# Performance work log

Hardware: AMD Instinct MI355X
Metric: run time of the kernel (lower is better)

## Reference

```python
import jax, jax.numpy as jnp
import numpy as np

BATCH, CHANNEL, LENGTH, CHI, D = 1024, 10, 784, 64, 2


def _dims():
    # dims[n+1] = min(d**(n+1), chi, d**(length-n-1)); dims[0] = 1
    dims = [1]
    for n in range(LENGTH):
        dims.append(min(D ** (n + 1), CHI, D ** (LENGTH - n - 1)))
    return dims


def _site_mask():
    # zero out tensor entries outside the [dims[n], dims[n+1]] bond block; this is
    # exactly equivalent to the per-site slicing in the torch code, but lets us
    # run one uniform lax.scan over sites with full-chi tensors.
    dims = _dims()
    mask = np.zeros((LENGTH, CHI, 1, CHI), np.float32)
    for n in range(LENGTH):
        mask[n, :dims[n], :, :dims[n + 1]] = 1.0
    return jnp.asarray(mask)


def setup_inputs() -> dict:
    key = jax.random.key(0)
    k1, k2 = jax.random.split(key)
    x = jax.random.uniform(k1, (BATCH, D, LENGTH), dtype=jnp.float32)
    scale = 1.0 / np.sqrt(CHI * D)
    tensors = jax.random.normal(k2, (CHANNEL, LENGTH, CHI, D, CHI), dtype=jnp.float32) * scale
    return {"x": x, "tensors": tensors}


def _forward(x, tensors):
    # mask == slicing tensors[:, nt, :dims[nt], :, :dims[nt+1]] at every site
    mt = tensors * _site_mask()[None]              # (c, L, chi, d, chi)
    A = jnp.transpose(mt, (1, 0, 2, 3, 4))         # (L, c, chi, d, chi)
    xs = jnp.transpose(x, (2, 0, 1))               # (L, n, d)
    is_last = jnp.arange(LENGTH) == LENGTH - 1
    y0 = jnp.zeros((x.shape[0], CHANNEL, CHI), x.dtype).at[:, :, 0].set(1.0)

    def step(y, inp):
        a, xv, last = inp
        y = jnp.einsum('nca,caib,ni->ncb', y, a, xv)
        # activation '(tanh(y)+1)/2' on all sites except the last one
        y = jnp.where(last, y, (jnp.tanh(y) + 1.0) * 0.5)
        return y, None

    y, _ = jax.lax.scan(step, y0, (A, xs, is_last))
    return y[:, :, :1]  # dims[length] == 1 -> (n, channel, 1)


def reference(x, tensors):
    return _forward(x, tensors)
```

## Files before the change

### kernel.cpp

```cpp
#include <hip/hip_runtime.h>
#include <hip/hip_bf16.h>


#define LEN 784
#define NCH 10

typedef short bf16x8 __attribute__((ext_vector_type(8)));
typedef float f32x4  __attribute__((ext_vector_type(4)));

#define WSA_SHORTS ((size_t)NCH * LEN * 8192)
#define WSX_FLOATS ((size_t)1024 * 2 * LEN)
#define WS_NEED (WSA_SHORTS * 2 + WSX_FLOATS * 4)

#define XSCALE -2.88539008177792681f
#define XUNDO  -0.34657359027997264f

static __device__ __forceinline__ unsigned short f2bf(float f) {
    union { __hip_bfloat16 h; unsigned short s; } u;
    u.h = __float2bfloat16(f);
    return u.s;
}

__global__ __launch_bounds__(1024) void prepass(const float* __restrict__ x,
                                                const float* __restrict__ tens,
                                                short* __restrict__ wsA,
                                                float* __restrict__ wsX)
{
    const int bid = blockIdx.x;
    const int t = threadIdx.x;
    if (bid < NCH * LEN) {
        const int w = t >> 8, ii = (t >> 7) & 1, kf = (t >> 6) & 1, l = t & 63;
        const int bout = 16 * w + (l & 15);
        const int a0 = 32 * kf + 8 * (l >> 4);
        const float* src = tens + (size_t)bid * 8192;
        unsigned int wv[4];
        #pragma unroll
        for (int p = 0; p < 4; ++p) {
            float f0 = src[(size_t)(a0 + 2 * p) * 128 + ii * 64 + bout];
            float f1 = src[(size_t)(a0 + 2 * p + 1) * 128 + ii * 64 + bout];
            wv[p] = (unsigned)f2bf(f0) | ((unsigned)f2bf(f1) << 16);
        }
        *(int4*)(wsA + (size_t)bid * 8192 + (size_t)t * 8) = *(int4*)wv;
    } else {
        int b = bid - NCH * LEN;
        if (t < LEN) {
            float v0 = x[(size_t)b * (2 * LEN) + t] * XSCALE;
            float v1 = x[(size_t)b * (2 * LEN) + LEN + t] * XSCALE;
            float2 pk; pk.x = v0; pk.y = v1;
            *(float2*)(wsX + (size_t)b * (2 * LEN) + 2 * t) = pk;
        }
    }
}

template <bool USE_WS>
__global__ __launch_bounds__(256, 3) void mps_fwd5(const float* __restrict__ x,
                                                   const float* __restrict__ tens,
                                                   const short* __restrict__ wsA,
                                                   const float* __restrict__ wsX,
                                                   float* __restrict__ out)
{
    __shared__ short tbuf[2][1024];

    const int tid = threadIdx.x;
    const int lane = tid & 63;
    const int w = tid >> 6;
    const int g = lane >> 4, l15 = lane & 15;

    const int p = blockIdx.x;
    const int gidx = (p & 7) * 80 + (p >> 3);
    const int ch = gidx >> 6;
    const int b0 = (gidx & 63) * 16;

    const short* asrc = wsA + (size_t)ch * LEN * 8192 + (size_t)w * 2048;
    const float* tsrc = tens + (size_t)ch * LEN * 8192;
    const float* xsrc = USE_WS ? (wsX + (size_t)(b0 + l15) * (2 * LEN))
                               : (x + (size_t)(b0 + l15) * (2 * LEN));

    for (int idx = tid; idx < 1024; idx += 256) {
        int col = idx >> 6, a = idx & 63;
        tbuf[0][col * 64 + 8 * ((a >> 3) ^ (col & 7)) + (a & 7)] =
            (a == 0) ? (short)0x3F80 : (short)0;
    }

    int rd_off0 = l15 * 64 + 8 * ((0 + g) ^ (l15 & 7));
    int rd_off1 = l15 * 64 + 8 * ((4 + g) ^ (l15 & 7));
    const int wr_off = l15 * 64 + 8 * ((2 * w + (g >> 1)) ^ (l15 & 7)) + 4 * (g & 1);

    auto loadA = [&](int site, bf16x8 (&A)[4]) {
        site = site < LEN ? site : LEN - 1;
        if (USE_WS) {
            const short* sb = asrc + (size_t)site * 8192;
            #pragma unroll
            for (int f = 0; f < 4; ++f)
                A[f] = *(const bf16x8*)(sb + f * 512 + lane * 8);
        } else {
            const float* sb = tsrc + (size_t)site * 8192;
            #pragma unroll
            for (int f = 0; f < 4; ++f) {
                int ii = f >> 1, kf = f & 1;
                int bout = 16 * w + l15;
                int a0 = 32 * kf + 8 * g;
                unsigned int wv[4];
                #pragma unroll
                for (int q2 = 0; q2 < 4; ++q2) {
                    float f0 = sb[(size_t)(a0 + 2 * q2) * 128 + ii * 64 + bout];
                    float f1 = sb[(size_t)(a0 + 2 * q2 + 1) * 128 + ii * 64 + bout];
                    wv[q2] = (unsigned)f2bf(f0) | ((unsigned)f2bf(f1) << 16);
                }
                A[f] = *(bf16x8*)wv;
            }
        }
    };

    auto loadX = [&](int nb, float4& qa, float4& qb) {
        nb = nb <= LEN - 4 ? nb : LEN - 4;
        if (USE_WS) {
            qa = *(const float4*)(xsrc + 2 * nb);
            qb = *(const float4*)(xsrc + 2 * nb + 4);
        } else {
            float4 xi0 = *(const float4*)(xsrc + nb);
            float4 xi1 = *(const float4*)(xsrc + LEN + nb);
            qa.x = xi0.x * XSCALE; qa.y = xi1.x * XSCALE;
            qa.z = xi0.y * XSCALE; qa.w = xi1.y * XSCALE;
            qb.x = xi0.z * XSCALE; qb.y = xi1.z * XSCALE;
            qb.z = xi0.w * XSCALE; qb.w = xi1.w * XSCALE;
        }
    };

    auto body = [&](int n, bf16x8 (&Ac)[4], bf16x8 (&Al)[4], float x0s, float x1s) {
        const int cur = n & 1, nxt = cur ^ 1;

        loadA(n + 2, Al);

        bf16x8 tf0 = *(const bf16x8*)&tbuf[cur][rd_off0];
        bf16x8 tf1 = *(const bf16x8*)&tbuf[cur][rd_off1];

        f32x4 acc0 = (f32x4){0.f, 0.f, 0.f, 0.f};
        f32x4 acc1 = (f32x4){0.f, 0.f, 0.f, 0.f};
        acc0 = __builtin_amdgcn_mfma_f32_16x16x32_bf16(Ac[0], tf0, acc0, 0, 0, 0);
        acc0 = __builtin_amdgcn_mfma_f32_16x16x32_bf16(Ac[1], tf1, acc0, 0, 0, 0);
        acc1 = __builtin_amdgcn_mfma_f32_16x16x32_bf16(Ac[2], tf0, acc1, 0, 0, 0);
        acc1 = __builtin_amdgcn_mfma_f32_16x16x32_bf16(Ac[3], tf1, acc1, 0, 0, 0);

        if (n == LEN - 1) {
            if (w == 0 && g == 0) {
                float v = (x0s * acc0[0] + x1s * acc1[0]) * XUNDO;
                out[(size_t)(b0 + l15) * NCH + ch] = v;
            }
        } else {
            int e1 = (n + 1) < 6 ? (1 << (n + 1)) : 64;
            int e2 = (783 - n) < 6 ? (1 << (783 - n)) : 64;
            int dout = e1 < e2 ? e1 : e2;
            int abase = 16 * w + 4 * g;
            unsigned short sv[4];
            #pragma unroll
            for (int r = 0; r < 4; ++r) {
                float u = x0s * acc0[r] + x1s * acc1[r];
                float sg = __builtin_amdgcn_rcpf(1.0f + exp2f(u));
                sv[r] = (abase + r < dout) ? f2bf(sg) : (unsigned short)0;
            }
            int2 pk;
            pk.x = (int)((unsigned)sv[0] | ((unsigned)sv[1] << 16));
            pk.y = (int)((unsigned)sv[2] | ((unsigned)sv[3] << 16));
            *(int2*)&tbuf[nxt][wr_off] = pk;
        }

        asm volatile("s_waitcnt lgkmcnt(0)\n\ts_barrier" ::: "memory");
    };

    __syncthreads();

    bf16x8 As0[4], As1[4], As2[4], As3[4];
    float4 xa, xb, xna, xnb;
    loadA(0, As0);
    loadA(1, As1);
    loadX(0, xa, xb);

    for (int nb = 0; nb < LEN; nb += 4) {
        loadX(nb + 4, xna, xnb);
        body(nb + 0, As0, As2, xa.x, xa.y);
        body(nb + 1, As1, As3, xa.z, xa.w);
        body(nb + 2, As2, As0, xb.x, xb.y);
        body(nb + 3, As3, As1, xb.z, xb.w);
        xa = xna; xb = xnb;
    }
}

extern "C" void kernel_launch(void* const* d_in, const int* in_sizes, int n_in,
                              void* d_out, int out_size, void* d_ws, size_t ws_size,
                              hipStream_t stream) {
    (void)in_sizes; (void)n_in; (void)out_size;
    const float* x    = (const float*)d_in[0];
    const float* tens = (const float*)d_in[1];
    float* out = (float*)d_out;
    if (ws_size >= WS_NEED) {
        short* wsA = (short*)d_ws;
        float* wsX = (float*)((char*)d_ws + WSA_SHORTS * 2);
        hipLaunchKernelGGL(prepass, dim3(NCH * LEN + 1024), dim3(1024), 0, stream,
                           x, tens, wsA, wsX);
        hipLaunchKernelGGL((mps_fwd5<true>), dim3(640), dim3(256), 0, stream,
                           x, tens, wsA, wsX, out);
    } else {
        hipLaunchKernelGGL((mps_fwd5<false>), dim3(640), dim3(256), 0, stream,
                           x, tens, (const short*)nullptr, (const float*)nullptr, out);
    }
}
```

Baseline: 554.2 us.

## Run each MPS chain in one wavefront, keeping state in registers without LDS or barriers

The kernel moves from four wavefronts per block, which shared the bond state through LDS with a barrier at every site, to a single 64-lane wavefront that computes all 64 output bonds itself. The prepass permutes the output-bond order so that the MFMA accumulator layout lines up with the B-operand register layout. The new state can then be fed straight back as the next site's operand, with no LDS round trip or s_barrier. The cost is four times more MFMA work and A-tile loads per wave (16 fragments, double-buffered, so much higher VGPR pressure). Only 640 waves are launched, so latency hiding and parallelism drop. Activation masking is also restricted to the boundary sites.

```diff
diff --git a/kernel.cpp b/kernel.cpp
--- a/kernel.cpp
+++ b/kernel.cpp
@@ -29,8 +29,9 @@
     const int bid = blockIdx.x;
     const int t = threadIdx.x;
     if (bid < NCH * LEN) {
-        const int w = t >> 8, ii = (t >> 7) & 1, kf = (t >> 6) & 1, l = t & 63;
-        const int bout = 16 * w + (l & 15);
+        const int mt = t >> 8, ii = (t >> 7) & 1, kf = (t >> 6) & 1, l = t & 63;
+        const int l15 = l & 15;
+        const int bout = 32 * (mt >> 1) + 8 * (l15 >> 2) + 4 * (mt & 1) + (l15 & 3);
         const int a0 = 32 * kf + 8 * (l >> 4);
         const float* src = tens + (size_t)bid * 8192;
         unsigned int wv[4];
@@ -53,17 +54,13 @@
 }
 
 template <bool USE_WS>
-__global__ __launch_bounds__(256, 3) void mps_fwd5(const float* __restrict__ x,
-                                                   const float* __restrict__ tens,
-                                                   const short* __restrict__ wsA,
-                                                   const float* __restrict__ wsX,
-                                                   float* __restrict__ out)
+__global__ __launch_bounds__(64) void mps_fwd6(const float* __restrict__ x,
+                                               const float* __restrict__ tens,
+                                               const short* __restrict__ wsA,
+                                               const float* __restrict__ wsX,
+                                               float* __restrict__ out)
 {
-    __shared__ short tbuf[2][1024];
-
-    const int tid = threadIdx.x;
-    const int lane = tid & 63;
-    const int w = tid >> 6;
+    const int lane = threadIdx.x;
     const int g = lane >> 4, l15 = lane & 15;
 
     const int p = blockIdx.x;
@@ -71,34 +68,29 @@
     const int ch = gidx >> 6;
     const int b0 = (gidx & 63) * 16;
 
-    const short* asrc = wsA + (size_t)ch * LEN * 8192 + (size_t)w * 2048;
+    const short* asrc = wsA + (size_t)ch * LEN * 8192;
     const float* tsrc = tens + (size_t)ch * LEN * 8192;
     const float* xsrc = USE_WS ? (wsX + (size_t)(b0 + l15) * (2 * LEN))
                                : (x + (size_t)(b0 + l15) * (2 * LEN));
 
-    for (int idx = tid; idx < 1024; idx += 256) {
-        int col = idx >> 6, a = idx & 63;
-        tbuf[0][col * 64 + 8 * ((a >> 3) ^ (col & 7)) + (a & 7)] =
-            (a == 0) ? (short)0x3F80 : (short)0;
-    }
-
-    int rd_off0 = l15 * 64 + 8 * ((0 + g) ^ (l15 & 7));
-    int rd_off1 = l15 * 64 + 8 * ((4 + g) ^ (l15 & 7));
-    const int wr_off = l15 * 64 + 8 * ((2 * w + (g >> 1)) ^ (l15 & 7)) + 4 * (g & 1);
-
-    auto loadA = [&](int site, bf16x8 (&A)[4]) {
+    bf16x8 tf0, tf1;
+    #pragma unroll
+    for (int j = 0; j < 8; ++j) { tf0[j] = 0; tf1[j] = 0; }
+    if (g == 0) tf0[0] = (short)0x3F80;
+
+    auto loadA = [&](int site, bf16x8 (&A)[16]) {
         site = site < LEN ? site : LEN - 1;
         if (USE_WS) {
             const short* sb = asrc + (size_t)site * 8192;
             #pragma unroll
-            for (int f = 0; f < 4; ++f)
+            for (int f = 0; f < 16; ++f)
                 A[f] = *(const bf16x8*)(sb + f * 512 + lane * 8);
         } else {
             const float* sb = tsrc + (size_t)site * 8192;
             #pragma unroll
-            for (int f = 0; f < 4; ++f) {
-                int ii = f >> 1, kf = f & 1;
-                int bout = 16 * w + l15;
+            for (int f = 0; f < 16; ++f) {
+                int mt = f >> 2, ii = (f >> 1) & 1, kf = f & 1;
+                int bout = 32 * (mt >> 1) + 8 * (l15 >> 2) + 4 * (mt & 1) + (l15 & 3);
                 int a0 = 32 * kf + 8 * g;
                 unsigned int wv[4];
                 #pragma unroll
@@ -127,61 +119,89 @@
         }
     };
 
-    auto body = [&](int n, bf16x8 (&Ac)[4], bf16x8 (&Al)[4], float x0s, float x1s) {
-        const int cur = n & 1, nxt = cur ^ 1;
-
-        loadA(n + 2, Al);
-
-        bf16x8 tf0 = *(const bf16x8*)&tbuf[cur][rd_off0];
-        bf16x8 tf1 = *(const bf16x8*)&tbuf[cur][rd_off1];
-
-        f32x4 acc0 = (f32x4){0.f, 0.f, 0.f, 0.f};
-        f32x4 acc1 = (f32x4){0.f, 0.f, 0.f, 0.f};
-        acc0 = __builtin_amdgcn_mfma_f32_16x16x32_bf16(Ac[0], tf0, acc0, 0, 0, 0);
-        acc0 = __builtin_amdgcn_mfma_f32_16x16x32_bf16(Ac[1], tf1, acc0, 0, 0, 0);
-        acc1 = __builtin_amdgcn_mfma_f32_16x16x32_bf16(Ac[2], tf0, acc1, 0, 0, 0);
-        acc1 = __builtin_amdgcn_mfma_f32_16x16x32_bf16(Ac[3], tf1, acc1, 0, 0, 0);
+    auto body = [&](int n, bf16x8 (&Ac)[16], bf16x8 (&An)[16], float x0s, float x1s) {
+        loadA(n + 1, An);
+
+        f32x4 acc[4][2];
+        #pragma unroll
+        for (int mt = 0; mt < 4; ++mt)
+            #pragma unroll
+            for (int ii = 0; ii < 2; ++ii)
+                acc[mt][ii] = (f32x4){0.f, 0.f, 0.f, 0.f};
+
+        #pragma unroll
+        for (int kf = 0; kf < 2; ++kf) {
+            bf16x8 tfk = kf ? tf1 : tf0;
+            #pragma unroll
+            for (int mt = 0; mt < 4; ++mt)
+                #pragma unroll
+                for (int ii = 0; ii < 2; ++ii)
+                    acc[mt][ii] = __builtin_amdgcn_mfma_f32_16x16x32_bf16(
+                        Ac[mt * 4 + ii * 2 + kf], tfk, acc[mt][ii], 0, 0, 0);
+        }
 
         if (n == LEN - 1) {
-            if (w == 0 && g == 0) {
-                float v = (x0s * acc0[0] + x1s * acc1[0]) * XUNDO;
+            if (g == 0) {
+                float v = (x0s * acc[0][0][0] + x1s * acc[0][1][0]) * XUNDO;
                 out[(size_t)(b0 + l15) * NCH + ch] = v;
             }
         } else {
-            int e1 = (n + 1) < 6 ? (1 << (n + 1)) : 64;
-            int e2 = (783 - n) < 6 ? (1 << (783 - n)) : 64;
-            int dout = e1 < e2 ? e1 : e2;
-            int abase = 16 * w + 4 * g;
-            unsigned short sv[4];
-            #pragma unroll
-            for (int r = 0; r < 4; ++r) {
-                float u = x0s * acc0[r] + x1s * acc1[r];
-                float sg = __builtin_amdgcn_rcpf(1.0f + exp2f(u));
-                sv[r] = (abase + r < dout) ? f2bf(sg) : (unsigned short)0;
+            unsigned pk[8];
+            bool masked = (n < 5) | (n > 777);
+            if (masked) {
+                int e1 = (n + 1) < 6 ? (1 << (n + 1)) : 64;
+                int e2 = (783 - n) < 6 ? (1 << (783 - n)) : 64;
+                int dout = e1 < e2 ? e1 : e2;
+                #pragma unroll
+                for (int mt = 0; mt < 4; ++mt) {
+                    int pb = 32 * (mt >> 1) + 8 * g + 4 * (mt & 1);
+                    #pragma unroll
+                    for (int rp = 0; rp < 2; ++rp) {
+                        unsigned short sv[2];
+                        #pragma unroll
+                        for (int q2 = 0; q2 < 2; ++q2) {
+                            int r = 2 * rp + q2;
+                            float u = x0s * acc[mt][0][r] + x1s * acc[mt][1][r];
+                            float sg = __builtin_amdgcn_rcpf(1.0f + exp2f(u));
+                            sv[q2] = (pb + r < dout) ? f2bf(sg) : (unsigned short)0;
+                        }
+                        pk[mt * 2 + rp] = (unsigned)sv[0] | ((unsigned)sv[1] << 16);
+                    }
+                }
+            } else {
+                #pragma unroll
+                for (int mt = 0; mt < 4; ++mt)
+                    #pragma unroll
+                    for (int rp = 0; rp < 2; ++rp) {
+                        unsigned short sv[2];
+                        #pragma unroll
+                        for (int q2 = 0; q2 < 2; ++q2) {
+                            int r = 2 * rp + q2;
+                            float u = x0s * acc[mt][0][r] + x1s * acc[mt][1][r];
+                            float sg = __builtin_amdgcn_rcpf(1.0f + exp2f(u));
+                            sv[q2] = f2bf(sg);
+                        }
+                        pk[mt * 2 + rp] = (unsigned)sv[0] | ((unsigned)sv[1] << 16);
+                    }
             }
-            int2 pk;
-            pk.x = (int)((unsigned)sv[0] | ((unsigned)sv[1] << 16));
-            pk.y = (int)((unsigned)sv[2] | ((unsigned)sv[3] << 16));
-            *(int2*)&tbuf[nxt][wr_off] = pk;
-        }
-
-        asm volatile("s_waitcnt lgkmcnt(0)\n\ts_barrier" ::: "memory");
+            union { unsigned u[4]; bf16x8 v; } u0, u1;
+            u0.u[0] = pk[0]; u0.u[1] = pk[1]; u0.u[2] = pk[2]; u0.u[3] = pk[3];
+            u1.u[0] = pk[4]; u1.u[1] = pk[5]; u1.u[2] = pk[6]; u1.u[3] = pk[7];
+            tf0 = u0.v; tf1 = u1.v;
+        }
     };
 
-    __syncthreads();
-
-    bf16x8 As0[4], As1[4], As2[4], As3[4];
+    bf16x8 A0[16], A1[16];
     float4 xa, xb, xna, xnb;
-    loadA(0, As0);
-    loadA(1, As1);
+    loadA(0, A0);
     loadX(0, xa, xb);
 
     for (int nb = 0; nb < LEN; nb += 4) {
         loadX(nb + 4, xna, xnb);
-        body(nb + 0, As0, As2, xa.x, xa.y);
-        body(nb + 1, As1, As3, xa.z, xa.w);
-        body(nb + 2, As2, As0, xb.x, xb.y);
-        body(nb + 3, As3, As1, xb.z, xb.w);
+        body(nb + 0, A0, A1, xa.x, xa.y);
+        body(nb + 1, A1, A0, xa.z, xa.w);
+        body(nb + 2, A0, A1, xb.x, xb.y);
+        body(nb + 3, A1, A0, xb.z, xb.w);
         xa = xna; xb = xnb;
     }
 }
@@ -198,10 +218,10 @@
         float* wsX = (float*)((char*)d_ws + WSA_SHORTS * 2);
         hipLaunchKernelGGL(prepass, dim3(NCH * LEN + 1024), dim3(1024), 0, stream,
                            x, tens, wsA, wsX);
-        hipLaunchKernelGGL((mps_fwd5<true>), dim3(640), dim3(256), 0, stream,
+        hipLaunchKernelGGL((mps_fwd6<true>), dim3(640), dim3(64), 0, stream,
                            x, tens, wsA, wsX, out);
     } else {
-        hipLaunchKernelGGL((mps_fwd5<false>), dim3(640), dim3(256), 0, stream,
+        hipLaunchKernelGGL((mps_fwd6<false>), dim3(640), dim3(64), 0, stream,
                            x, tens, (const short*)nullptr, (const float*)nullptr, out);
     }
 }
```

After: 990.8 us. 78.8% more time.
